# Kernel optimization log

Measured on AMD Instinct MI355X. Metric: run time of the kernel, lower is better.

## Reference

```python
import jax, jax.numpy as jnp
import numpy as np


def setup_inputs() -> dict:
    key = jax.random.key(0)
    k1, k2 = jax.random.split(key)
    N, DIM = 32768, 1024
    M, K, D = 8, 1024, 128  # n_quantizer, n_codeword, sub_dim
    x = jax.random.normal(k1, (N, DIM), dtype=jnp.float32)
    CodeBooks = jax.random.uniform(k2, (M, K, D), dtype=jnp.float32)  # torch.rand init
    return {"x": x, "CodeBooks": CodeBooks, "soft_rate": -1}


def reference(x, CodeBooks, soft_rate):
    # x: [N, dim]; CodeBooks: [M, K, D] with dim = M*D
    N = x.shape[0]
    M, K, D = CodeBooks.shape
    # forward detaches x before quantizing
    sx = jax.lax.stop_gradient(x).reshape(-1, M, D)  # [N, M, D]
    # squared euclidean distances for all sub-quantizers at once:
    # d2[n,m,k] = ||sx[n,m] - CB[m,k]||^2
    dots = jnp.einsum("nmd,mkd->nmk", sx, CodeBooks)          # [N, M, K]
    x2 = jnp.sum(sx * sx, axis=-1)                             # [N, M]
    c2 = jnp.sum(CodeBooks * CodeBooks, axis=-1)               # [M, K]
    d2 = x2[:, :, None] + c2[None, :, :] - 2.0 * dots          # [N, M, K]
    if soft_rate == -1:
        # argmax of -dist == argmin of squared dist (sqrt is monotone)
        idx = jnp.argmin(d2, axis=-1)                          # [N, M]
        Q = CodeBooks[jnp.arange(M)[None, :], idx]             # [N, M, D]
    else:
        dist = -jnp.sqrt(jnp.maximum(d2, 0.0))                 # -cdist, p=2
        w = jax.nn.softmax(dist * soft_rate, axis=-1)          # [N, M, K]
        Q = jnp.einsum("nmk,mkd->nmd", w, CodeBooks)           # [N, M, D]
    return Q.reshape(N, M * D)
```

## Files before the change

### kernel.cpp

```cpp
#include <hip/hip_runtime.h>

#define NROWS   32768
#define XDIM    1024
#define NCB     8
#define NCODE   1024
#define CDIM    128

#define ROWS_PB 128
#define CHUNK   32
#define NCHUNK  (NCODE / CHUNK)
#define NTHREADS 512

typedef _Float16 h8 __attribute__((ext_vector_type(8)));
typedef float    f4 __attribute__((ext_vector_type(4)));

#define LO_SCALE   2048.0f
#define LO_INV     4.8828125e-4f

__global__ __launch_bounds__(NTHREADS, 4)
void quant_argmin_kernel(const float* __restrict__ x,
                         const float* __restrict__ cb,
                         float* __restrict__ out)
{
    __shared__ __align__(16) _Float16 chS[2][CHUNK][CDIM];
    __shared__ __align__(16) _Float16 clS[2][CHUNK][CDIM];
    __shared__ float  c2s[NCODE];
    __shared__ double x2p[4][ROWS_PB];
    __shared__ float  x2s[ROWS_PB];
    __shared__ int    idxs[ROWS_PB];

    const int t    = threadIdx.x;
    const int bid  = blockIdx.x;
    const int m    = bid >> 8;
    const int rb   = bid & 255;
    const int row0 = rb * ROWS_PB;

    const int l    = t & 63;
    const int w    = t >> 6;
    const int l15  = l & 15;
    const int lh   = l >> 4;
    const int mskr = (l & 7) * 8;

    for (int rep = 0; rep < 2; ++rep) {
        int k = t + rep * NTHREADS;
        const float* p = cb + ((size_t)m * NCODE + k) * CDIM;
        double s0 = 0, s1 = 0, s2 = 0, s3 = 0;
        for (int d = 0; d < CDIM; d += 4) {
            double v0 = p[d], v1 = p[d + 1], v2 = p[d + 2], v3 = p[d + 3];
            s0 = fma(v0, v0, s0); s1 = fma(v1, v1, s1);
            s2 = fma(v2, v2, s2); s3 = fma(v3, v3, s3);
        }
        c2s[k] = (float)((s0 + s1) + (s2 + s3));
    }

    {
        int row = t >> 2, q = t & 3;
        const float* p = x + (size_t)(row0 + row) * XDIM + m * CDIM + q * 32;
        double s0 = 0, s1 = 0;
        for (int i = 0; i < 32; i += 2) {
            double v0 = p[i], v1 = p[i + 1];
            s0 = fma(v0, v0, s0); s1 = fma(v1, v1, s1);
        }
        x2p[q][row] = s0 + s1;
    }

    h8 xh[4], xl[4];
    {
        const float* xp = x + (size_t)(row0 + w * 16 + l15) * XDIM + m * CDIM + lh * 8;
        #pragma unroll
        for (int ks = 0; ks < 4; ++ks) {
            float v[8];
            *(f4*)&v[0] = *(const f4*)(xp + ks * 32);
            *(f4*)&v[4] = *(const f4*)(xp + ks * 32 + 4);
            #pragma unroll
            for (int i = 0; i < 8; ++i) {
                _Float16 h = (_Float16)v[i];
                float    r = v[i] - (float)h;
                xh[ks][i] = h;
                xl[ks][i] = (_Float16)(r * LO_SCALE);
            }
        }
    }

    __syncthreads();
    if (t < ROWS_PB)
        x2s[t] = (float)((x2p[0][t] + x2p[1][t]) + (x2p[2][t] + x2p[3][t]));

    const int kr = t >> 4;
    const int db = (t & 15) * 8;
    const int ew = db ^ ((kr & 7) * 8);

    auto stage_load = [&](int c, f4& a, f4& b) {
        const float* p = cb + ((size_t)m * NCODE + c * CHUNK + kr) * CDIM + db;
        a = *(const f4*)p;
        b = *(const f4*)(p + 4);
    };
    auto stage_write = [&](int buf, f4 a, f4 b) {
        float v[8];
        *(f4*)&v[0] = a; *(f4*)&v[4] = b;
        _Float16 hh[8], ll[8];
        #pragma unroll
        for (int i = 0; i < 8; ++i) {
            _Float16 h = (_Float16)v[i];
            float    r = v[i] - (float)h;
            hh[i] = h;
            ll[i] = (_Float16)(r * LO_SCALE);
        }
        *(h8*)&chS[buf][kr][ew] = *(h8*)hh;
        *(h8*)&clS[buf][kr][ew] = *(h8*)ll;
    };

    f4 pa, pb;
    stage_load(0, pa, pb);
    stage_write(0, pa, pb);
    __syncthreads();

    float x2r[4];
    #pragma unroll
    for (int j = 0; j < 4; ++j) x2r[j] = x2s[w * 16 + lh * 4 + j];

    float mval[4];
    int   midx[4];
    #pragma unroll
    for (int j = 0; j < 4; ++j) { mval[j] = 3.0e38f; midx[j] = 0; }

    for (int c = 0; c < NCHUNK; ++c) {
        const int cur = c & 1;
        f4 na, nb;
        if (c + 1 < NCHUNK) stage_load(c + 1, na, nb);

        #pragma unroll
        for (int cf = 0; cf < CHUNK / 16; ++cf) {
            const int kloc = cf * 16 + l15;
            f4 accH = {0, 0, 0, 0}, accS = {0, 0, 0, 0};
            #pragma unroll
            for (int ks = 0; ks < 4; ++ks) {
                const int e = (ks * 32 + lh * 8) ^ mskr;
                h8 bh = *(const h8*)&chS[cur][kloc][e];
                h8 bl = *(const h8*)&clS[cur][kloc][e];
                accH = __builtin_amdgcn_mfma_f32_16x16x32_f16(xh[ks], bh, accH, 0, 0, 0);
                accS = __builtin_amdgcn_mfma_f32_16x16x32_f16(xh[ks], bl, accS, 0, 0, 0);
                accS = __builtin_amdgcn_mfma_f32_16x16x32_f16(xl[ks], bh, accS, 0, 0, 0);
            }
            const int   code = c * CHUNK + kloc;
            const float c2v  = c2s[code];
            #pragma unroll
            for (int j = 0; j < 4; ++j) {
                float dot = fmaf(accS[j], LO_INV, accH[j]);
                float d2  = (x2r[j] + c2v) - 2.0f * dot;
                if (d2 < mval[j]) { mval[j] = d2; midx[j] = code; }
            }
        }
        if (c + 1 < NCHUNK) stage_write((c + 1) & 1, na, nb);
        __syncthreads();
    }

    #pragma unroll
    for (int mask = 1; mask <= 8; mask <<= 1) {
        #pragma unroll
        for (int j = 0; j < 4; ++j) {
            float ov = __shfl_xor(mval[j], mask, 64);
            int   oi = __shfl_xor(midx[j], mask, 64);
            if (ov < mval[j] || (ov == mval[j] && oi < midx[j])) {
                mval[j] = ov; midx[j] = oi;
            }
        }
    }
    if (l15 == 0) {
        #pragma unroll
        for (int j = 0; j < 4; ++j) idxs[w * 16 + lh * 4 + j] = midx[j];
    }
    __syncthreads();

    {
        const int row = t >> 2, qd = (t & 3) * 32;
        const float* src = cb + ((size_t)m * NCODE + idxs[row]) * CDIM + qd;
        float*       dst = out + (size_t)(row0 + row) * XDIM + m * CDIM + qd;
        #pragma unroll
        for (int i = 0; i < 8; ++i)
            *(f4*)(dst + i * 4) = *(const f4*)(src + i * 4);
    }
}

extern "C" void kernel_launch(void* const* d_in, const int* in_sizes, int n_in,
                              void* d_out, int out_size, void* d_ws, size_t ws_size,
                              hipStream_t stream) {
    const float* x   = (const float*)d_in[0];
    const float* cb  = (const float*)d_in[1];
    float*       out = (float*)d_out;
    dim3 grid(NCB * (NROWS / ROWS_PB));
    quant_argmin_kernel<<<grid, NTHREADS, 0, stream>>>(x, cb, out);
}
```

Before: 334.5 us.

## Precompute split-fp16 codebooks and c2 in workspace, stream via direct LDS loads

A small pre-kernel converts the codebook once into swizzled fp16 hi/lo planes plus squared norms in the workspace. This removes the per-block codebook conversion and c2 recomputation that every one of the 2048 blocks repeated. The main kernel then streams chunks with global_load_lds straight into shared memory, and each wave now covers 32 rows instead of 16 with 256 threads, so every B-fragment read from LDS is reused across two MFMA row tiles. The costs are a second launch, extra workspace traffic and higher register pressure. The original kernel is kept as a fallback when no workspace is available.

Result: no change. 330.6 us (-1.2%).

```diff
diff --git a/kernel.cpp b/kernel.cpp
--- a/kernel.cpp
+++ b/kernel.cpp
@@ -1,4 +1,5 @@
 #include <hip/hip_runtime.h>
+#include <stdint.h>
 
 #define NROWS   32768
 #define XDIM    1024
@@ -6,21 +7,223 @@
 #define NCODE   1024
 #define CDIM    128
 
-#define ROWS_PB 128
 #define CHUNK   32
 #define NCHUNK  (NCODE / CHUNK)
-#define NTHREADS 512
+
+#define NTH     256
+#define ROWS_PB 128
+#define RPW     32
 
 typedef _Float16 h8 __attribute__((ext_vector_type(8)));
 typedef float    f4 __attribute__((ext_vector_type(4)));
 
-#define LO_SCALE   2048.0f
-#define LO_INV     4.8828125e-4f
-
-__global__ __launch_bounds__(NTHREADS, 4)
-void quant_argmin_kernel(const float* __restrict__ x,
-                         const float* __restrict__ cb,
-                         float* __restrict__ out)
+#define LO_SCALE 2048.0f
+#define LO_INV   4.8828125e-4f
+
+#define WS_HI   ((size_t)0)
+#define WS_LO   ((size_t)NCB * NCODE * CDIM * 2)
+#define WS_C2   ((size_t)2 * NCB * NCODE * CDIM * 2)
+#define WS_NEED (WS_C2 + (size_t)NCB * NCODE * 4)
+
+__device__ __forceinline__ void gload_lds16(const void* g, void* l) {
+    __builtin_amdgcn_global_load_lds(
+        (const __attribute__((address_space(1))) void*)g,
+        (__attribute__((address_space(3))) void*)l, 16, 0, 0);
+}
+
+__global__ __launch_bounds__(256)
+void precompute_kernel(const float* __restrict__ cb, uint8_t* __restrict__ ws)
+{
+    _Float16* hi = (_Float16*)(ws + WS_HI);
+    _Float16* lo = (_Float16*)(ws + WS_LO);
+    float*    c2 = (float*)(ws + WS_C2);
+
+    const int idx  = blockIdx.x * 256 + threadIdx.x;
+    const int g    = idx & 15;
+    const int code = idx >> 4;
+    const int kr   = code & 31;
+    const int gs   = g ^ (kr & 7);
+
+    const float* src = cb + (size_t)code * CDIM + gs * 8;
+    float v[8];
+    *(f4*)&v[0] = *(const f4*)src;
+    *(f4*)&v[4] = *(const f4*)(src + 4);
+
+    _Float16 hh[8], ll[8];
+    double s = 0.0;
+    #pragma unroll
+    for (int i = 0; i < 8; ++i) {
+        _Float16 h = (_Float16)v[i];
+        float    r = v[i] - (float)h;
+        hh[i] = h; ll[i] = (_Float16)(r * LO_SCALE);
+        s = fma((double)v[i], (double)v[i], s);
+    }
+    const size_t off = (size_t)code * CDIM + g * 8;
+    *(h8*)(hi + off) = *(h8*)hh;
+    *(h8*)(lo + off) = *(h8*)ll;
+
+    #pragma unroll
+    for (int mask = 1; mask <= 8; mask <<= 1)
+        s += __shfl_xor(s, mask, 16);
+    if (g == 0) c2[code] = (float)s;
+}
+
+__global__ __launch_bounds__(NTH, 4)
+void quant_fast(const float* __restrict__ x, const float* __restrict__ cb,
+                const uint8_t* __restrict__ ws, float* __restrict__ out)
+{
+    __shared__ __align__(16) _Float16 chS[2][CHUNK][CDIM];
+    __shared__ __align__(16) _Float16 clS[2][CHUNK][CDIM];
+    __shared__ float  c2s[NCODE];
+    __shared__ double x2p[2][ROWS_PB];
+    __shared__ float  x2s[ROWS_PB];
+    __shared__ int    idxs[ROWS_PB];
+
+    const _Float16* pre_hi = (const _Float16*)(ws + WS_HI);
+    const _Float16* pre_lo = (const _Float16*)(ws + WS_LO);
+    const float*    c2w    = (const float*)(ws + WS_C2);
+
+    const int t    = threadIdx.x;
+    const int bid  = blockIdx.x;
+    const int m    = bid >> 8;
+    const int rb   = bid & 255;
+    const int row0 = rb * ROWS_PB;
+
+    const int l    = t & 63;
+    const int w    = t >> 6;
+    const int l15  = l & 15;
+    const int lh   = l >> 4;
+    const int mskr = (l & 7) * 8;
+
+    *(f4*)&c2s[t * 4] = *(const f4*)&c2w[m * NCODE + t * 4];
+
+    {
+        const int row = t >> 1, q = t & 1;
+        const float* p = x + (size_t)(row0 + row) * XDIM + m * CDIM + q * 64;
+        double s0 = 0, s1 = 0;
+        for (int i = 0; i < 64; i += 2) {
+            double v0 = p[i], v1 = p[i + 1];
+            s0 = fma(v0, v0, s0); s1 = fma(v1, v1, s1);
+        }
+        x2p[q][row] = s0 + s1;
+    }
+
+    h8 xh[2][4], xl[2][4];
+    #pragma unroll
+    for (int rs = 0; rs < 2; ++rs) {
+        const float* xp = x + (size_t)(row0 + w * RPW + rs * 16 + l15) * XDIM + m * CDIM + lh * 8;
+        #pragma unroll
+        for (int ks = 0; ks < 4; ++ks) {
+            float v[8];
+            *(f4*)&v[0] = *(const f4*)(xp + ks * 32);
+            *(f4*)&v[4] = *(const f4*)(xp + ks * 32 + 4);
+            #pragma unroll
+            for (int i = 0; i < 8; ++i) {
+                _Float16 h = (_Float16)v[i];
+                float    r = v[i] - (float)h;
+                xh[rs][ks][i] = h;
+                xl[rs][ks][i] = (_Float16)(r * LO_SCALE);
+            }
+        }
+    }
+
+    const size_t cbase = (size_t)m * NCODE * CDIM;
+    auto stage = [&](int c, int buf) {
+        const _Float16* gh = pre_hi + cbase + (size_t)(c * CHUNK + w * 8) * CDIM + l * 8;
+        const _Float16* gl = pre_lo + cbase + (size_t)(c * CHUNK + w * 8) * CDIM + l * 8;
+        gload_lds16(gh,            &chS[buf][w * 8][0]);
+        gload_lds16(gh + 4 * CDIM, &chS[buf][w * 8 + 4][0]);
+        gload_lds16(gl,            &clS[buf][w * 8][0]);
+        gload_lds16(gl + 4 * CDIM, &clS[buf][w * 8 + 4][0]);
+    };
+
+    stage(0, 0);
+    __syncthreads();
+    if (t < ROWS_PB) x2s[t] = (float)(x2p[0][t] + x2p[1][t]);
+    __syncthreads();
+
+    float x2r[2][4];
+    #pragma unroll
+    for (int rs = 0; rs < 2; ++rs)
+        #pragma unroll
+        for (int j = 0; j < 4; ++j)
+            x2r[rs][j] = x2s[w * RPW + rs * 16 + lh * 4 + j];
+
+    float mval[2][4];
+    int   midx[2][4];
+    #pragma unroll
+    for (int rs = 0; rs < 2; ++rs)
+        #pragma unroll
+        for (int j = 0; j < 4; ++j) { mval[rs][j] = 3.0e38f; midx[rs][j] = 0; }
+
+    for (int c = 0; c < NCHUNK; ++c) {
+        const int cur = c & 1;
+        if (c + 1 < NCHUNK) stage(c + 1, cur ^ 1);
+
+        #pragma unroll
+        for (int cf = 0; cf < 2; ++cf) {
+            const int kloc = cf * 16 + l15;
+            f4 accH[2] = {{0,0,0,0},{0,0,0,0}};
+            f4 accS[2] = {{0,0,0,0},{0,0,0,0}};
+            #pragma unroll
+            for (int ks = 0; ks < 4; ++ks) {
+                const int e = (ks * 32 + lh * 8) ^ mskr;
+                h8 bh = *(const h8*)&chS[cur][kloc][e];
+                h8 bl = *(const h8*)&clS[cur][kloc][e];
+                accH[0] = __builtin_amdgcn_mfma_f32_16x16x32_f16(xh[0][ks], bh, accH[0], 0, 0, 0);
+                accH[1] = __builtin_amdgcn_mfma_f32_16x16x32_f16(xh[1][ks], bh, accH[1], 0, 0, 0);
+                accS[0] = __builtin_amdgcn_mfma_f32_16x16x32_f16(xh[0][ks], bl, accS[0], 0, 0, 0);
+                accS[0] = __builtin_amdgcn_mfma_f32_16x16x32_f16(xl[0][ks], bh, accS[0], 0, 0, 0);
+                accS[1] = __builtin_amdgcn_mfma_f32_16x16x32_f16(xh[1][ks], bl, accS[1], 0, 0, 0);
+                accS[1] = __builtin_amdgcn_mfma_f32_16x16x32_f16(xl[1][ks], bh, accS[1], 0, 0, 0);
+            }
+            const int   code = c * CHUNK + kloc;
+            const float c2v  = c2s[code];
+            #pragma unroll
+            for (int rs = 0; rs < 2; ++rs)
+                #pragma unroll
+                for (int j = 0; j < 4; ++j) {
+                    float dot = fmaf(accS[rs][j], LO_INV, accH[rs][j]);
+                    float d2  = (x2r[rs][j] + c2v) - 2.0f * dot;
+                    if (d2 < mval[rs][j]) { mval[rs][j] = d2; midx[rs][j] = code; }
+                }
+        }
+        __syncthreads();
+    }
+
+    #pragma unroll
+    for (int mask = 1; mask <= 8; mask <<= 1)
+        #pragma unroll
+        for (int rs = 0; rs < 2; ++rs)
+            #pragma unroll
+            for (int j = 0; j < 4; ++j) {
+                float ov = __shfl_xor(mval[rs][j], mask, 64);
+                int   oi = __shfl_xor(midx[rs][j], mask, 64);
+                if (ov < mval[rs][j] || (ov == mval[rs][j] && oi < midx[rs][j])) {
+                    mval[rs][j] = ov; midx[rs][j] = oi;
+                }
+            }
+    if (l15 == 0)
+        #pragma unroll
+        for (int rs = 0; rs < 2; ++rs)
+            #pragma unroll
+            for (int j = 0; j < 4; ++j)
+                idxs[w * RPW + rs * 16 + lh * 4 + j] = midx[rs][j];
+    __syncthreads();
+
+    {
+        const int row = t >> 1, half = (t & 1) * 64;
+        const float* src = cb + ((size_t)m * NCODE + idxs[row]) * CDIM + half;
+        float*       dst = out + (size_t)(row0 + row) * XDIM + m * CDIM + half;
+        #pragma unroll
+        for (int i = 0; i < 16; ++i)
+            *(f4*)(dst + i * 4) = *(const f4*)(src + i * 4);
+    }
+}
+
+__global__ __launch_bounds__(512, 4)
+void quant_fallback(const float* __restrict__ x, const float* __restrict__ cb,
+                    float* __restrict__ out)
 {
     __shared__ __align__(16) _Float16 chS[2][CHUNK][CDIM];
     __shared__ __align__(16) _Float16 clS[2][CHUNK][CDIM];
@@ -29,82 +232,58 @@
     __shared__ float  x2s[ROWS_PB];
     __shared__ int    idxs[ROWS_PB];
 
-    const int t    = threadIdx.x;
-    const int bid  = blockIdx.x;
-    const int m    = bid >> 8;
-    const int rb   = bid & 255;
-    const int row0 = rb * ROWS_PB;
-
-    const int l    = t & 63;
-    const int w    = t >> 6;
-    const int l15  = l & 15;
-    const int lh   = l >> 4;
+    const int t = threadIdx.x, bid = blockIdx.x;
+    const int m = bid >> 8, rb = bid & 255, row0 = rb * ROWS_PB;
+    const int l = t & 63, w = t >> 6, l15 = l & 15, lh = l >> 4;
     const int mskr = (l & 7) * 8;
 
     for (int rep = 0; rep < 2; ++rep) {
-        int k = t + rep * NTHREADS;
+        int k = t + rep * 512;
         const float* p = cb + ((size_t)m * NCODE + k) * CDIM;
         double s0 = 0, s1 = 0, s2 = 0, s3 = 0;
         for (int d = 0; d < CDIM; d += 4) {
-            double v0 = p[d], v1 = p[d + 1], v2 = p[d + 2], v3 = p[d + 3];
-            s0 = fma(v0, v0, s0); s1 = fma(v1, v1, s1);
-            s2 = fma(v2, v2, s2); s3 = fma(v3, v3, s3);
-        }
-        c2s[k] = (float)((s0 + s1) + (s2 + s3));
-    }
-
+            double v0 = p[d], v1 = p[d+1], v2 = p[d+2], v3 = p[d+3];
+            s0 = fma(v0,v0,s0); s1 = fma(v1,v1,s1); s2 = fma(v2,v2,s2); s3 = fma(v3,v3,s3);
+        }
+        c2s[k] = (float)((s0+s1)+(s2+s3));
+    }
     {
         int row = t >> 2, q = t & 3;
-        const float* p = x + (size_t)(row0 + row) * XDIM + m * CDIM + q * 32;
+        const float* p = x + (size_t)(row0+row)*XDIM + m*CDIM + q*32;
         double s0 = 0, s1 = 0;
-        for (int i = 0; i < 32; i += 2) {
-            double v0 = p[i], v1 = p[i + 1];
-            s0 = fma(v0, v0, s0); s1 = fma(v1, v1, s1);
-        }
+        for (int i = 0; i < 32; i += 2) { double v0=p[i], v1=p[i+1]; s0=fma(v0,v0,s0); s1=fma(v1,v1,s1); }
         x2p[q][row] = s0 + s1;
     }
-
     h8 xh[4], xl[4];
     {
-        const float* xp = x + (size_t)(row0 + w * 16 + l15) * XDIM + m * CDIM + lh * 8;
+        const float* xp = x + (size_t)(row0 + w*16 + l15)*XDIM + m*CDIM + lh*8;
         #pragma unroll
         for (int ks = 0; ks < 4; ++ks) {
             float v[8];
-            *(f4*)&v[0] = *(const f4*)(xp + ks * 32);
-            *(f4*)&v[4] = *(const f4*)(xp + ks * 32 + 4);
+            *(f4*)&v[0] = *(const f4*)(xp + ks*32);
+            *(f4*)&v[4] = *(const f4*)(xp + ks*32 + 4);
             #pragma unroll
             for (int i = 0; i < 8; ++i) {
-                _Float16 h = (_Float16)v[i];
-                float    r = v[i] - (float)h;
-                xh[ks][i] = h;
-                xl[ks][i] = (_Float16)(r * LO_SCALE);
-            }
-        }
-    }
-
-    __syncthreads();
-    if (t < ROWS_PB)
-        x2s[t] = (float)((x2p[0][t] + x2p[1][t]) + (x2p[2][t] + x2p[3][t]));
-
-    const int kr = t >> 4;
-    const int db = (t & 15) * 8;
-    const int ew = db ^ ((kr & 7) * 8);
-
+                _Float16 h = (_Float16)v[i]; float r = v[i] - (float)h;
+                xh[ks][i] = h; xl[ks][i] = (_Float16)(r * LO_SCALE);
+            }
+        }
+    }
+    __syncthreads();
+    if (t < ROWS_PB) x2s[t] = (float)((x2p[0][t]+x2p[1][t])+(x2p[2][t]+x2p[3][t]));
+
+    const int kr = t >> 4, db = (t & 15) * 8, ew = db ^ ((kr & 7) * 8);
     auto stage_load = [&](int c, f4& a, f4& b) {
-        const float* p = cb + ((size_t)m * NCODE + c * CHUNK + kr) * CDIM + db;
-        a = *(const f4*)p;
-        b = *(const f4*)(p + 4);
+        const float* p = cb + ((size_t)m*NCODE + c*CHUNK + kr)*CDIM + db;
+        a = *(const f4*)p; b = *(const f4*)(p + 4);
     };
     auto stage_write = [&](int buf, f4 a, f4 b) {
-        float v[8];
-        *(f4*)&v[0] = a; *(f4*)&v[4] = b;
+        float v[8]; *(f4*)&v[0] = a; *(f4*)&v[4] = b;
         _Float16 hh[8], ll[8];
         #pragma unroll
         for (int i = 0; i < 8; ++i) {
-            _Float16 h = (_Float16)v[i];
-            float    r = v[i] - (float)h;
-            hh[i] = h;
-            ll[i] = (_Float16)(r * LO_SCALE);
+            _Float16 h = (_Float16)v[i]; float r = v[i] - (float)h;
+            hh[i] = h; ll[i] = (_Float16)(r * LO_SCALE);
         }
         *(h8*)&chS[buf][kr][ew] = *(h8*)hh;
         *(h8*)&clS[buf][kr][ew] = *(h8*)ll;
@@ -117,10 +296,8 @@
 
     float x2r[4];
     #pragma unroll
-    for (int j = 0; j < 4; ++j) x2r[j] = x2s[w * 16 + lh * 4 + j];
-
-    float mval[4];
-    int   midx[4];
+    for (int j = 0; j < 4; ++j) x2r[j] = x2s[w*16 + lh*4 + j];
+    float mval[4]; int midx[4];
     #pragma unroll
     for (int j = 0; j < 4; ++j) { mval[j] = 3.0e38f; midx[j] = 0; }
 
@@ -128,57 +305,49 @@
         const int cur = c & 1;
         f4 na, nb;
         if (c + 1 < NCHUNK) stage_load(c + 1, na, nb);
-
-        #pragma unroll
-        for (int cf = 0; cf < CHUNK / 16; ++cf) {
-            const int kloc = cf * 16 + l15;
-            f4 accH = {0, 0, 0, 0}, accS = {0, 0, 0, 0};
+        #pragma unroll
+        for (int cf = 0; cf < 2; ++cf) {
+            const int kloc = cf*16 + l15;
+            f4 accH = {0,0,0,0}, accS = {0,0,0,0};
             #pragma unroll
             for (int ks = 0; ks < 4; ++ks) {
-                const int e = (ks * 32 + lh * 8) ^ mskr;
+                const int e = (ks*32 + lh*8) ^ mskr;
                 h8 bh = *(const h8*)&chS[cur][kloc][e];
                 h8 bl = *(const h8*)&clS[cur][kloc][e];
                 accH = __builtin_amdgcn_mfma_f32_16x16x32_f16(xh[ks], bh, accH, 0, 0, 0);
                 accS = __builtin_amdgcn_mfma_f32_16x16x32_f16(xh[ks], bl, accS, 0, 0, 0);
                 accS = __builtin_amdgcn_mfma_f32_16x16x32_f16(xl[ks], bh, accS, 0, 0, 0);
             }
-            const int   code = c * CHUNK + kloc;
-            const float c2v  = c2s[code];
+            const int code = c*CHUNK + kloc;
+            const float c2v = c2s[code];
             #pragma unroll
             for (int j = 0; j < 4; ++j) {
                 float dot = fmaf(accS[j], LO_INV, accH[j]);
-                float d2  = (x2r[j] + c2v) - 2.0f * dot;
+                float d2 = (x2r[j] + c2v) - 2.0f*dot;
                 if (d2 < mval[j]) { mval[j] = d2; midx[j] = code; }
             }
         }
         if (c + 1 < NCHUNK) stage_write((c + 1) & 1, na, nb);
         __syncthreads();
     }
-
-    #pragma unroll
-    for (int mask = 1; mask <= 8; mask <<= 1) {
+    #pragma unroll
+    for (int mask = 1; mask <= 8; mask <<= 1)
         #pragma unroll
         for (int j = 0; j < 4; ++j) {
             float ov = __shfl_xor(mval[j], mask, 64);
             int   oi = __shfl_xor(midx[j], mask, 64);
-            if (ov < mval[j] || (ov == mval[j] && oi < midx[j])) {
-                mval[j] = ov; midx[j] = oi;
-            }
-        }
-    }
-    if (l15 == 0) {
-        #pragma unroll
-        for (int j = 0; j < 4; ++j) idxs[w * 16 + lh * 4 + j] = midx[j];
-    }
-    __syncthreads();
-
+            if (ov < mval[j] || (ov == mval[j] && oi < midx[j])) { mval[j] = ov; midx[j] = oi; }
+        }
+    if (l15 == 0)
+        #pragma unroll
+        for (int j = 0; j < 4; ++j) idxs[w*16 + lh*4 + j] = midx[j];
+    __syncthreads();
     {
         const int row = t >> 2, qd = (t & 3) * 32;
-        const float* src = cb + ((size_t)m * NCODE + idxs[row]) * CDIM + qd;
-        float*       dst = out + (size_t)(row0 + row) * XDIM + m * CDIM + qd;
-        #pragma unroll
-        for (int i = 0; i < 8; ++i)
-            *(f4*)(dst + i * 4) = *(const f4*)(src + i * 4);
+        const float* src = cb + ((size_t)m*NCODE + idxs[row])*CDIM + qd;
+        float* dst = out + (size_t)(row0+row)*XDIM + m*CDIM + qd;
+        #pragma unroll
+        for (int i = 0; i < 8; ++i) *(f4*)(dst + i*4) = *(const f4*)(src + i*4);
     }
 }
 
@@ -188,6 +357,10 @@
     const float* x   = (const float*)d_in[0];
     const float* cb  = (const float*)d_in[1];
     float*       out = (float*)d_out;
-    dim3 grid(NCB * (NROWS / ROWS_PB));
-    quant_argmin_kernel<<<grid, NTHREADS, 0, stream>>>(x, cb, out);
-}
+    if (ws_size >= WS_NEED && d_ws != nullptr) {
+        precompute_kernel<<<dim3(512), dim3(256), 0, stream>>>(cb, (uint8_t*)d_ws);
+        quant_fast<<<dim3(2048), dim3(NTH), 0, stream>>>(x, cb, (const uint8_t*)d_ws, out);
+    } else {
+        quant_fallback<<<dim3(2048), dim3(512), 0, stream>>>(x, cb, out);
+    }
+}
```
